# Kernel optimization log

Hardware: AMD Instinct MI355X
Metric: run time of the kernel (lower is better)

## Reference

```python
import jax, jax.numpy as jnp
import numpy as np

K = 16  # knn_graph k, loop=True (self included since d(i,i)=0 is minimal)


def _knn_idx(pos, k):
    # exact kNN via pairwise squared distances; [N, k] neighbor indices
    sq = jnp.sum(pos * pos, axis=-1)
    d2 = sq[:, None] + sq[None, :] - 2.0 * (pos @ pos.T)  # [N, N]
    _, idx = jax.lax.top_k(-d2, k)
    return idx


def _pointnet_conv(x, pos, idx, Wa, ba, Wb, bb):
    # PointNetConv: msg = MLP(concat(x_j, pos_j - pos_i)), max-aggregate over neighbors
    rel = pos[idx] - pos[:, None, :]                    # [N, K, 3]
    m = jnp.concatenate([x[idx], rel], axis=-1)          # [N, K, Cin+3]
    h = jax.nn.relu(m @ Wa + ba) @ Wb + bb               # [N, K, Cout]
    return jnp.max(h, axis=1)                            # [N, Cout]


def setup_inputs() -> dict:
    key = jax.random.key(0)
    ks = jax.random.split(key, 13)
    N = 8192
    c1, c2, c3 = 64, 64, 128
    s = lambda fi: 1.0 / np.sqrt(fi)
    pos = jax.random.normal(ks[0], (N, 3), dtype=jnp.float32)
    return {
        "pos": pos,
        "W1a": jax.random.normal(ks[1], (3 + 3, c1), jnp.float32) * s(6),
        "b1a": jnp.zeros((c1,), jnp.float32),
        "W1b": jax.random.normal(ks[2], (c1, c1), jnp.float32) * s(c1),
        "b1b": jnp.zeros((c1,), jnp.float32),
        "W2a": jax.random.normal(ks[3], (c1 + 3, c2), jnp.float32) * s(c1 + 3),
        "b2a": jnp.zeros((c2,), jnp.float32),
        "W2b": jax.random.normal(ks[4], (c2, c2), jnp.float32) * s(c2),
        "b2b": jnp.zeros((c2,), jnp.float32),
        "W3a": jax.random.normal(ks[5], (c2 + 3, c3), jnp.float32) * s(c2 + 3),
        "b3a": jnp.zeros((c3,), jnp.float32),
        "W3b": jax.random.normal(ks[6], (c3, c3), jnp.float32) * s(c3),
        "b3b": jnp.zeros((c3,), jnp.float32),
    }


def reference(pos, W1a, b1a, W1b, b1b, W2a, b2a, W2b, b2b, W3a, b3a, W3b, b3b):
    idx = _knn_idx(pos, K)
    h1 = jax.nn.relu(_pointnet_conv(pos, pos, idx, W1a, b1a, W1b, b1b))
    h2 = jax.nn.relu(_pointnet_conv(h1, pos, idx, W2a, b2a, W2b, b2b))
    h3 = jax.nn.relu(_pointnet_conv(h2, pos, idx, W3a, b3a, W3b, b3b))
    return (h1, h2, h3)
```

## Files before the change

kernel.cpp:

```cpp
#include <hip/hip_runtime.h>
#include <math.h>

#define N_PTS 8192
#define KNN 16

typedef __attribute__((ext_vector_type(8))) short bf16x8;
typedef __attribute__((ext_vector_type(4))) float f32x4v;

__device__ __forceinline__ unsigned short f2bf(float f)
{
    unsigned u = __float_as_uint(f);
    u = u + 0x7fffu + ((u >> 16) & 1u);
    return (unsigned short)(u >> 16);
}
__device__ __forceinline__ unsigned pack2(float a, float b)
{
    return (unsigned)f2bf(a) | ((unsigned)f2bf(b) << 16);
}
__device__ __forceinline__ float rfl(float x)
{
    return __int_as_float(__builtin_amdgcn_readfirstlane(__float_as_int(x)));
}

__global__ __launch_bounds__(256) void prep_kernel(const float* __restrict__ pos,
                                                   float4* __restrict__ pos4)
{
    const int i = blockIdx.x * 256 + threadIdx.x;
    const float x = pos[i * 3 + 0];
    const float y = pos[i * 3 + 1];
    const float z = pos[i * 3 + 2];
    pos4[i] = make_float4(x, y, z, fmaf(x, x, fmaf(y, y, z * z)));
}

__global__ __launch_bounds__(64) void prep_weights(
    const float* __restrict__ w1a, const float* __restrict__ w1b,
    const float* __restrict__ w2a, const float* __restrict__ w2b,
    const float* __restrict__ w3a, const float* __restrict__ w3b,
    uint4* __restrict__ dst)
{
    const float* Ws[6] = {w1a, w1b, w2a, w2b, w3a, w3b};
    const int Kd[6] = {6, 64, 67, 64, 67, 128};
    const int Nd[6] = {64, 64, 64, 64, 128, 128};
    const int start[7] = {0, 4, 12, 24, 32, 56, 88};

    const int b = blockIdx.x;
    int m = 0;
    while (b >= start[m + 1]) ++m;
    const int f  = b - start[m];
    const int NT = Nd[m] / 16;
    const int ks = f / NT, nt = f % NT;

    const int lane = threadIdx.x;
    const int c  = nt * 16 + (lane & 15);
    const int k0 = ks * 32 + (lane >> 4) * 8;
    const int K = Kd[m], N = Nd[m];
    const float* W = Ws[m];

    float v[8];
#pragma unroll
    for (int j = 0; j < 8; ++j) {
        const int kk = k0 + j;
        v[j] = (kk < K) ? W[kk * N + c] : 0.0f;
    }
    uint4 o;
    o.x = pack2(v[0], v[1]); o.y = pack2(v[2], v[3]);
    o.z = pack2(v[4], v[5]); o.w = pack2(v[6], v[7]);
    dst[b * 64 + lane] = o;
}

__device__ __forceinline__ unsigned sortkey(const float d2)
{
    unsigned u = __float_as_uint(d2);
    u ^= (unsigned)((int)u >> 31) | 0x80000000u;
    return u;
}

constexpr int CAP = 128;
constexpr int QB  = 8;
constexpr int QW  = QB / 4;

__global__ __launch_bounds__(256) void knn_kernel(const float4* __restrict__ pos4,
                                                  int* __restrict__ idx_out)
{
    __shared__ float mins[QB][4][64];
    __shared__ float Ts[QB];
    __shared__ unsigned long long surv[QB][CAP];
    __shared__ int scnt[QB];

    const int tid   = threadIdx.x;
    const int w     = tid >> 6;
    const int lane  = tid & 63;
    const int qbase = blockIdx.x * QB;
    const int cbase = w * (N_PTS / 4);

    if (tid < QB) scnt[tid] = 0;

    float qx[QB], qy[QB], qz[QB];
#pragma unroll
    for (int qi = 0; qi < QB; ++qi) {
        const float4 qp = pos4[qbase + qi];
        qx[qi] = rfl(-2.0f * qp.x);
        qy[qi] = rfl(-2.0f * qp.y);
        qz[qi] = rfl(-2.0f * qp.z);
    }

    float mn[QB];
#pragma unroll
    for (int qi = 0; qi < QB; ++qi) mn[qi] = 1e30f;

#pragma unroll 4
    for (int t = 0; t < N_PTS / 4 / 64; ++t) {
        const float4 p = pos4[cbase + t * 64 + lane];
#pragma unroll
        for (int qi = 0; qi < QB; ++qi) {
            const float s = fmaf(qx[qi], p.x, fmaf(qy[qi], p.y, fmaf(qz[qi], p.z, p.w)));
            mn[qi] = fminf(mn[qi], s);
        }
    }
#pragma unroll
    for (int qi = 0; qi < QB; ++qi) mins[qi][w][lane] = mn[qi];
    __syncthreads();

#pragma unroll
    for (int k = 0; k < QW; ++k) {
        const int q = w * QW + k;
        float v = fminf(fminf(mins[q][0][lane], mins[q][1][lane]),
                        fminf(mins[q][2][lane], mins[q][3][lane]));
#pragma unroll
        for (int kk = 2; kk <= 64; kk <<= 1)
#pragma unroll
            for (int j = kk >> 1; j > 0; j >>= 1) {
                const float o = __shfl_xor(v, j);
                const bool up = ((lane & kk) == 0);
                const bool lo = ((lane & j) == 0);
                v = (up == lo) ? fminf(v, o) : fmaxf(v, o);
            }
        if (lane == 15) Ts[q] = v;
    }
    __syncthreads();

    float T[QB];
#pragma unroll
    for (int qi = 0; qi < QB; ++qi) T[qi] = rfl(Ts[qi]);

#pragma unroll 4
    for (int t = 0; t < N_PTS / 4 / 64; ++t) {
        const int j = cbase + t * 64 + lane;
        const float4 p = pos4[j];
#pragma unroll
        for (int qi = 0; qi < QB; ++qi) {
            const float s = fmaf(qx[qi], p.x, fmaf(qy[qi], p.y, fmaf(qz[qi], p.z, p.w)));
            if (s <= T[qi]) {
                const int slot = atomicAdd(&scnt[qi], 1);
                if (slot < CAP)
                    surv[qi][slot] = ((unsigned long long)sortkey(s) << 32) | (unsigned)j;
            }
        }
    }
    __syncthreads();

    for (int k = 0; k < QW; ++k) {
        const int q = w * QW + k;
        const int n = min(scnt[q], CAP);
        const unsigned long long k0 = (lane < n) ? surv[q][lane] : ~0ull;
        const unsigned long long k1 = (lane + 64 < n) ? surv[q][lane + 64] : ~0ull;
        int r0 = 0, r1 = 0;
        for (int e = 0; e < n; ++e) {
            const unsigned long long ke = surv[q][e];
            r0 += (ke < k0) ? 1 : 0;
            r1 += (ke < k1) ? 1 : 0;
        }
        if (lane < n && r0 < KNN)
            idx_out[(qbase + q) * KNN + r0] = (int)(unsigned)(k0 & 0xFFFFFFFFu);
        if (lane + 64 < n && r1 < KNN)
            idx_out[(qbase + q) * KNN + r1] = (int)(unsigned)(k1 & 0xFFFFFFFFu);
    }
}

template <int CIN, int CMID, int COUT, int WM, int WN>
__global__ __launch_bounds__(256) void conv_mfma(
    const float* __restrict__ x, const float* __restrict__ pos,
    const int* __restrict__ idx,
    const uint4* __restrict__ fA, const float* __restrict__ ba,
    const uint4* __restrict__ fB, const float* __restrict__ bb,
    float* __restrict__ out)
{
    constexpr int PB  = 8, M = 128;
    constexpr int K1  = (CIN + 3 + 31) & ~31;
    constexpr int KS1 = K1 / 32;
    constexpr int KP1 = K1 + 8;
    constexpr int KS2 = CMID / 32;
    constexpr int KP2 = CMID + 8;
    constexpr int NT  = COUT / 16;
    constexpr int NTW = NT / WN;
    constexpr int MFW = (M / 16) / WM;

    __shared__ unsigned short msg[M][KP1];
    __shared__ unsigned short hbuf[M][KP2];
    __shared__ int nbr[M];

    const int tid  = threadIdx.x;
    const int lane = tid & 63;
    const int w    = tid >> 6;
    const int wm   = w / WN, wn = w % WN;
    const int i0   = blockIdx.x * PB;

    if (tid < M) nbr[tid] = idx[i0 * KNN + tid];
    __syncthreads();

    if constexpr (CIN == 3) {
        if (tid < M) {
            const int row = tid, p = row >> 4, j = nbr[row];
            const float ax = pos[j * 3 + 0], ay = pos[j * 3 + 1], az = pos[j * 3 + 2];
            const float bx = pos[(i0 + p) * 3 + 0], by = pos[(i0 + p) * 3 + 1],
                        bz = pos[(i0 + p) * 3 + 2];
            uint4 c0;
            c0.x = pack2(ax, ay);
            c0.y = pack2(az, ax - bx);
            c0.z = pack2(ay - by, az - bz);
            c0.w = 0u;
            *reinterpret_cast<uint4*>(&msg[row][0]) = c0;
            const uint4 z = make_uint4(0, 0, 0, 0);
            *reinterpret_cast<uint4*>(&msg[row][8])  = z;
            *reinterpret_cast<uint4*>(&msg[row][16]) = z;
            *reinterpret_cast<uint4*>(&msg[row][24]) = z;
        }
    } else {
        const int row = tid >> 1, hh = tid & 1;
        const int j = nbr[row];
        const float* xr = x + j * CIN + hh * 32;
#pragma unroll
        for (int cc = 0; cc < 32; cc += 8) {
            const float4 f0 = *reinterpret_cast<const float4*>(xr + cc);
            const float4 f1 = *reinterpret_cast<const float4*>(xr + cc + 4);
            uint4 o;
            o.x = pack2(f0.x, f0.y); o.y = pack2(f0.z, f0.w);
            o.z = pack2(f1.x, f1.y); o.w = pack2(f1.z, f1.w);
            *reinterpret_cast<uint4*>(&msg[row][hh * 32 + cc]) = o;
        }
        if (hh) {
            const int p = row >> 4;
            const float rx = pos[j * 3 + 0] - pos[(i0 + p) * 3 + 0];
            const float ry = pos[j * 3 + 1] - pos[(i0 + p) * 3 + 1];
            const float rz = pos[j * 3 + 2] - pos[(i0 + p) * 3 + 2];
            uint4 c0;
            c0.x = pack2(rx, ry);
            c0.y = pack2(rz, 0.0f);
            c0.z = 0u; c0.w = 0u;
            *reinterpret_cast<uint4*>(&msg[row][64]) = c0;
            const uint4 z = make_uint4(0, 0, 0, 0);
            *reinterpret_cast<uint4*>(&msg[row][72]) = z;
            *reinterpret_cast<uint4*>(&msg[row][80]) = z;
            *reinterpret_cast<uint4*>(&msg[row][88]) = z;
        }
    }
    __syncthreads();

    {
        uint4 b1[KS1][NTW];
#pragma unroll
        for (int ks = 0; ks < KS1; ++ks)
#pragma unroll
            for (int nt = 0; nt < NTW; ++nt)
                b1[ks][nt] = fA[(ks * NT + wn * NTW + nt) * 64 + lane];

        f32x4v acc[MFW][NTW];
#pragma unroll
        for (int mf = 0; mf < MFW; ++mf)
#pragma unroll
            for (int nt = 0; nt < NTW; ++nt) acc[mf][nt] = (f32x4v)0.0f;

#pragma unroll
        for (int mf = 0; mf < MFW; ++mf) {
            bf16x8 a[KS1];
#pragma unroll
            for (int ks = 0; ks < KS1; ++ks)
                a[ks] = *reinterpret_cast<const bf16x8*>(
                    &msg[(wm * MFW + mf) * 16 + (lane & 15)][ks * 32 + (lane >> 4) * 8]);
#pragma unroll
            for (int nt = 0; nt < NTW; ++nt)
#pragma unroll
                for (int ks = 0; ks < KS1; ++ks)
                    acc[mf][nt] = __builtin_amdgcn_mfma_f32_16x16x32_bf16(
                        a[ks], __builtin_bit_cast(bf16x8, b1[ks][nt]), acc[mf][nt], 0, 0, 0);
        }

        float bav[NTW];
#pragma unroll
        for (int nt = 0; nt < NTW; ++nt) bav[nt] = ba[(wn * NTW + nt) * 16 + (lane & 15)];

#pragma unroll
        for (int mf = 0; mf < MFW; ++mf)
#pragma unroll
            for (int nt = 0; nt < NTW; ++nt)
#pragma unroll
                for (int r = 0; r < 4; ++r) {
                    const float v = fmaxf(acc[mf][nt][r] + bav[nt], 0.0f);
                    hbuf[(wm * MFW + mf) * 16 + (lane >> 4) * 4 + r]
                        [(wn * NTW + nt) * 16 + (lane & 15)] = f2bf(v);
                }
    }
    __syncthreads();

    {
        uint4 b2[KS2][NTW];
#pragma unroll
        for (int ks = 0; ks < KS2; ++ks)
#pragma unroll
            for (int nt = 0; nt < NTW; ++nt)
                b2[ks][nt] = fB[(ks * NT + wn * NTW + nt) * 64 + lane];

        f32x4v acc[MFW][NTW];
#pragma unroll
        for (int mf = 0; mf < MFW; ++mf)
#pragma unroll
            for (int nt = 0; nt < NTW; ++nt) acc[mf][nt] = (f32x4v)0.0f;

#pragma unroll
        for (int mf = 0; mf < MFW; ++mf) {
            bf16x8 a[KS2];
#pragma unroll
            for (int ks = 0; ks < KS2; ++ks)
                a[ks] = *reinterpret_cast<const bf16x8*>(
                    &hbuf[(wm * MFW + mf) * 16 + (lane & 15)][ks * 32 + (lane >> 4) * 8]);
#pragma unroll
            for (int nt = 0; nt < NTW; ++nt)
#pragma unroll
                for (int ks = 0; ks < KS2; ++ks)
                    acc[mf][nt] = __builtin_amdgcn_mfma_f32_16x16x32_bf16(
                        a[ks], __builtin_bit_cast(bf16x8, b2[ks][nt]), acc[mf][nt], 0, 0, 0);
        }

        float bbv[NTW];
#pragma unroll
        for (int nt = 0; nt < NTW; ++nt) bbv[nt] = bb[(wn * NTW + nt) * 16 + (lane & 15)];

#pragma unroll
        for (int mf = 0; mf < MFW; ++mf)
#pragma unroll
            for (int nt = 0; nt < NTW; ++nt) {
                const f32x4v t = acc[mf][nt];
                float m0 = fmaxf(fmaxf(t[0], t[1]), fmaxf(t[2], t[3]));
                m0 = fmaxf(m0, __shfl_xor(m0, 16));
                m0 = fmaxf(m0, __shfl_xor(m0, 32));
                const float v = fmaxf(m0 + bbv[nt], 0.0f);
                if (lane < 16)
                    out[(i0 + wm * MFW + mf) * COUT + (wn * NTW + nt) * 16 + lane] = v;
            }
    }
}

extern "C" void kernel_launch(void* const* d_in, const int* in_sizes, int n_in,
                              void* d_out, int out_size, void* d_ws, size_t ws_size,
                              hipStream_t stream)
{
    const float* pos = (const float*)d_in[0];
    const float* W1a = (const float*)d_in[1];
    const float* b1a = (const float*)d_in[2];
    const float* W1b = (const float*)d_in[3];
    const float* b1b = (const float*)d_in[4];
    const float* W2a = (const float*)d_in[5];
    const float* b2a = (const float*)d_in[6];
    const float* W2b = (const float*)d_in[7];
    const float* b2b = (const float*)d_in[8];
    const float* W3a = (const float*)d_in[9];
    const float* b3a = (const float*)d_in[10];
    const float* W3b = (const float*)d_in[11];
    const float* b3b = (const float*)d_in[12];

    float* out = (float*)d_out;
    float* h1 = out;
    float* h2 = out + N_PTS * 64;
    float* h3 = out + N_PTS * 128;

    int*   idx     = (int*)d_ws;
    uint4* wsFrags = (uint4*)((char*)d_ws + N_PTS * KNN * 4);

    float4* pos4 = (float4*)h3;

    prep_weights<<<88, 64, 0, stream>>>(W1a, W1b, W2a, W2b, W3a, W3b, wsFrags);
    prep_kernel<<<N_PTS / 256, 256, 0, stream>>>(pos, pos4);
    knn_kernel<<<N_PTS / QB, 256, 0, stream>>>(pos4, idx);

    const uint4* fW1a = wsFrags + 0 * 64;
    const uint4* fW1b = wsFrags + 4 * 64;
    const uint4* fW2a = wsFrags + 12 * 64;
    const uint4* fW2b = wsFrags + 24 * 64;
    const uint4* fW3a = wsFrags + 32 * 64;
    const uint4* fW3b = wsFrags + 56 * 64;

    conv_mfma<3, 64, 64, 4, 1><<<N_PTS / 8, 256, 0, stream>>>(
        pos, pos, idx, fW1a, b1a, fW1b, b1b, h1);
    conv_mfma<64, 64, 64, 4, 1><<<N_PTS / 8, 256, 0, stream>>>(
        h1, pos, idx, fW2a, b2a, fW2b, b2b, h2);
    conv_mfma<64, 128, 128, 2, 2><<<N_PTS / 8, 256, 0, stream>>>(
        h2, pos, idx, fW3a, b3a, fW3b, b3b, h3);
}
```

Baseline: 78.55 us.

## Merge prep kernels, double kNN query batch, prefetch candidates, alias conv LDS buffers

Combines the weight-fragment and pos4 prep kernels into one launch to save a kernel launch. Raises the kNN queries per block from 8 to 16 so each candidate load is reused across more queries, and software-prefetches candidate points four at a time in both kNN passes. In the conv kernel the msg and hbuf LDS arrays share one buffer, separated by an extra barrier, which cuts LDS use and may raise occupancy. The larger query batch adds register pressure and halves the kNN grid size.

```diff
diff --git a/kernel.cpp b/kernel.cpp
--- a/kernel.cpp
+++ b/kernel.cpp
@@ -22,50 +22,47 @@
     return __int_as_float(__builtin_amdgcn_readfirstlane(__float_as_int(x)));
 }
 
-__global__ __launch_bounds__(256) void prep_kernel(const float* __restrict__ pos,
-                                                   float4* __restrict__ pos4)
-{
-    const int i = blockIdx.x * 256 + threadIdx.x;
-    const float x = pos[i * 3 + 0];
-    const float y = pos[i * 3 + 1];
-    const float z = pos[i * 3 + 2];
-    pos4[i] = make_float4(x, y, z, fmaf(x, x, fmaf(y, y, z * z)));
-}
-
-__global__ __launch_bounds__(64) void prep_weights(
+__global__ __launch_bounds__(256) void prep_all(
+    const float* __restrict__ pos, float4* __restrict__ pos4,
     const float* __restrict__ w1a, const float* __restrict__ w1b,
     const float* __restrict__ w2a, const float* __restrict__ w2b,
     const float* __restrict__ w3a, const float* __restrict__ w3b,
     uint4* __restrict__ dst)
 {
-    const float* Ws[6] = {w1a, w1b, w2a, w2b, w3a, w3b};
-    const int Kd[6] = {6, 64, 67, 64, 67, 128};
-    const int Nd[6] = {64, 64, 64, 64, 128, 128};
-    const int start[7] = {0, 4, 12, 24, 32, 56, 88};
-
     const int b = blockIdx.x;
-    int m = 0;
-    while (b >= start[m + 1]) ++m;
-    const int f  = b - start[m];
-    const int NT = Nd[m] / 16;
-    const int ks = f / NT, nt = f % NT;
-
-    const int lane = threadIdx.x;
-    const int c  = nt * 16 + (lane & 15);
-    const int k0 = ks * 32 + (lane >> 4) * 8;
-    const int K = Kd[m], N = Nd[m];
-    const float* W = Ws[m];
-
-    float v[8];
-#pragma unroll
-    for (int j = 0; j < 8; ++j) {
-        const int kk = k0 + j;
-        v[j] = (kk < K) ? W[kk * N + c] : 0.0f;
-    }
-    uint4 o;
-    o.x = pack2(v[0], v[1]); o.y = pack2(v[2], v[3]);
-    o.z = pack2(v[4], v[5]); o.w = pack2(v[6], v[7]);
-    dst[b * 64 + lane] = o;
+    if (b < 88) {
+        if (threadIdx.x >= 64) return;
+        const float* Ws[6] = {w1a, w1b, w2a, w2b, w3a, w3b};
+        const int Kd[6] = {6, 64, 67, 64, 67, 128};
+        const int Nd[6] = {64, 64, 64, 64, 128, 128};
+        const int start[7] = {0, 4, 12, 24, 32, 56, 88};
+        int m = 0;
+        while (b >= start[m + 1]) ++m;
+        const int f  = b - start[m];
+        const int NT = Nd[m] / 16;
+        const int ks = f / NT, nt = f % NT;
+        const int lane = threadIdx.x;
+        const int c  = nt * 16 + (lane & 15);
+        const int k0 = ks * 32 + (lane >> 4) * 8;
+        const int K = Kd[m], N = Nd[m];
+        const float* W = Ws[m];
+        float v[8];
+#pragma unroll
+        for (int j = 0; j < 8; ++j) {
+            const int kk = k0 + j;
+            v[j] = (kk < K) ? W[kk * N + c] : 0.0f;
+        }
+        uint4 o;
+        o.x = pack2(v[0], v[1]); o.y = pack2(v[2], v[3]);
+        o.z = pack2(v[4], v[5]); o.w = pack2(v[6], v[7]);
+        dst[b * 64 + lane] = o;
+    } else {
+        const int i = (b - 88) * 256 + threadIdx.x;
+        const float x = pos[i * 3 + 0];
+        const float y = pos[i * 3 + 1];
+        const float z = pos[i * 3 + 2];
+        pos4[i] = make_float4(x, y, z, fmaf(x, x, fmaf(y, y, z * z)));
+    }
 }
 
 __device__ __forceinline__ unsigned sortkey(const float d2)
@@ -76,7 +73,7 @@
 }
 
 constexpr int CAP = 128;
-constexpr int QB  = 8;
+constexpr int QB  = 16;
 constexpr int QW  = QB / 4;
 
 __global__ __launch_bounds__(256) void knn_kernel(const float4* __restrict__ pos4,
@@ -108,13 +105,31 @@
 #pragma unroll
     for (int qi = 0; qi < QB; ++qi) mn[qi] = 1e30f;
 
-#pragma unroll 4
-    for (int t = 0; t < N_PTS / 4 / 64; ++t) {
-        const float4 p = pos4[cbase + t * 64 + lane];
+    const float4* cp = pos4 + cbase + lane;
+
+    {
+        float4 c0 = cp[0 * 64], c1 = cp[1 * 64], c2 = cp[2 * 64], c3 = cp[3 * 64];
+#pragma unroll 1
+        for (int t = 0; t < 28; t += 4) {
+            const float4 n0 = cp[(t + 4) * 64];
+            const float4 n1 = cp[(t + 5) * 64];
+            const float4 n2 = cp[(t + 6) * 64];
+            const float4 n3 = cp[(t + 7) * 64];
+#pragma unroll
+            for (int qi = 0; qi < QB; ++qi) {
+                mn[qi] = fminf(mn[qi], fmaf(qx[qi], c0.x, fmaf(qy[qi], c0.y, fmaf(qz[qi], c0.z, c0.w))));
+                mn[qi] = fminf(mn[qi], fmaf(qx[qi], c1.x, fmaf(qy[qi], c1.y, fmaf(qz[qi], c1.z, c1.w))));
+                mn[qi] = fminf(mn[qi], fmaf(qx[qi], c2.x, fmaf(qy[qi], c2.y, fmaf(qz[qi], c2.z, c2.w))));
+                mn[qi] = fminf(mn[qi], fmaf(qx[qi], c3.x, fmaf(qy[qi], c3.y, fmaf(qz[qi], c3.z, c3.w))));
+            }
+            c0 = n0; c1 = n1; c2 = n2; c3 = n3;
+        }
 #pragma unroll
         for (int qi = 0; qi < QB; ++qi) {
-            const float s = fmaf(qx[qi], p.x, fmaf(qy[qi], p.y, fmaf(qz[qi], p.z, p.w)));
-            mn[qi] = fminf(mn[qi], s);
+            mn[qi] = fminf(mn[qi], fmaf(qx[qi], c0.x, fmaf(qy[qi], c0.y, fmaf(qz[qi], c0.z, c0.w))));
+            mn[qi] = fminf(mn[qi], fmaf(qx[qi], c1.x, fmaf(qy[qi], c1.y, fmaf(qz[qi], c1.z, c1.w))));
+            mn[qi] = fminf(mn[qi], fmaf(qx[qi], c2.x, fmaf(qy[qi], c2.y, fmaf(qz[qi], c2.z, c2.w))));
+            mn[qi] = fminf(mn[qi], fmaf(qx[qi], c3.x, fmaf(qy[qi], c3.y, fmaf(qz[qi], c3.z, c3.w))));
         }
     }
 #pragma unroll
@@ -143,18 +158,30 @@
 #pragma unroll
     for (int qi = 0; qi < QB; ++qi) T[qi] = rfl(Ts[qi]);
 
-#pragma unroll 4
-    for (int t = 0; t < N_PTS / 4 / 64; ++t) {
-        const int j = cbase + t * 64 + lane;
-        const float4 p = pos4[j];
-#pragma unroll
-        for (int qi = 0; qi < QB; ++qi) {
-            const float s = fmaf(qx[qi], p.x, fmaf(qy[qi], p.y, fmaf(qz[qi], p.z, p.w)));
-            if (s <= T[qi]) {
-                const int slot = atomicAdd(&scnt[qi], 1);
-                if (slot < CAP)
-                    surv[qi][slot] = ((unsigned long long)sortkey(s) << 32) | (unsigned)j;
+    {
+        float4 c0 = cp[0 * 64], c1 = cp[1 * 64], c2 = cp[2 * 64], c3 = cp[3 * 64];
+#pragma unroll 1
+        for (int t = 0; t < 32; t += 4) {
+            float4 n0, n1, n2, n3;
+            if (t + 4 < 32) {
+                n0 = cp[(t + 4) * 64]; n1 = cp[(t + 5) * 64];
+                n2 = cp[(t + 6) * 64]; n3 = cp[(t + 7) * 64];
             }
+#pragma unroll
+            for (int u = 0; u < 4; ++u) {
+                const float4 p = (u == 0) ? c0 : (u == 1) ? c1 : (u == 2) ? c2 : c3;
+                const int j = cbase + (t + u) * 64 + lane;
+#pragma unroll
+                for (int qi = 0; qi < QB; ++qi) {
+                    const float s = fmaf(qx[qi], p.x, fmaf(qy[qi], p.y, fmaf(qz[qi], p.z, p.w)));
+                    if (s <= T[qi]) {
+                        const int slot = atomicAdd(&scnt[qi], 1);
+                        if (slot < CAP)
+                            surv[qi][slot] = ((unsigned long long)sortkey(s) << 32) | (unsigned)j;
+                    }
+                }
+            }
+            if (t + 4 < 32) { c0 = n0; c1 = n1; c2 = n2; c3 = n3; }
         }
     }
     __syncthreads();
@@ -194,10 +221,12 @@
     constexpr int NT  = COUT / 16;
     constexpr int NTW = NT / WN;
     constexpr int MFW = (M / 16) / WM;
-
-    __shared__ unsigned short msg[M][KP1];
-    __shared__ unsigned short hbuf[M][KP2];
+    constexpr int MSGS = M * KP1;
+    constexpr int HBS  = M * KP2;
+    constexpr int BUFS = (MSGS > HBS) ? MSGS : HBS;
+
     __shared__ int nbr[M];
+    __shared__ __align__(16) unsigned short buf[BUFS];
 
     const int tid  = threadIdx.x;
     const int lane = tid & 63;
@@ -219,11 +248,11 @@
             c0.y = pack2(az, ax - bx);
             c0.z = pack2(ay - by, az - bz);
             c0.w = 0u;
-            *reinterpret_cast<uint4*>(&msg[row][0]) = c0;
+            *reinterpret_cast<uint4*>(&buf[row * KP1 + 0])  = c0;
             const uint4 z = make_uint4(0, 0, 0, 0);
-            *reinterpret_cast<uint4*>(&msg[row][8])  = z;
-            *reinterpret_cast<uint4*>(&msg[row][16]) = z;
-            *reinterpret_cast<uint4*>(&msg[row][24]) = z;
+            *reinterpret_cast<uint4*>(&buf[row * KP1 + 8])  = z;
+            *reinterpret_cast<uint4*>(&buf[row * KP1 + 16]) = z;
+            *reinterpret_cast<uint4*>(&buf[row * KP1 + 24]) = z;
         }
     } else {
         const int row = tid >> 1, hh = tid & 1;
@@ -236,7 +265,7 @@
             uint4 o;
             o.x = pack2(f0.x, f0.y); o.y = pack2(f0.z, f0.w);
             o.z = pack2(f1.x, f1.y); o.w = pack2(f1.z, f1.w);
-            *reinterpret_cast<uint4*>(&msg[row][hh * 32 + cc]) = o;
+            *reinterpret_cast<uint4*>(&buf[row * KP1 + hh * 32 + cc]) = o;
         }
         if (hh) {
             const int p = row >> 4;
@@ -247,15 +276,16 @@
             c0.x = pack2(rx, ry);
             c0.y = pack2(rz, 0.0f);
             c0.z = 0u; c0.w = 0u;
-            *reinterpret_cast<uint4*>(&msg[row][64]) = c0;
+            *reinterpret_cast<uint4*>(&buf[row * KP1 + 64]) = c0;
             const uint4 z = make_uint4(0, 0, 0, 0);
-            *reinterpret_cast<uint4*>(&msg[row][72]) = z;
-            *reinterpret_cast<uint4*>(&msg[row][80]) = z;
-            *reinterpret_cast<uint4*>(&msg[row][88]) = z;
-        }
-    }
-    __syncthreads();
-
+            *reinterpret_cast<uint4*>(&buf[row * KP1 + 72]) = z;
+            *reinterpret_cast<uint4*>(&buf[row * KP1 + 80]) = z;
+            *reinterpret_cast<uint4*>(&buf[row * KP1 + 88]) = z;
+        }
+    }
+    __syncthreads();
+
+    f32x4v acc[MFW][NTW];
     {
         uint4 b1[KS1][NTW];
 #pragma unroll
@@ -264,7 +294,6 @@
             for (int nt = 0; nt < NTW; ++nt)
                 b1[ks][nt] = fA[(ks * NT + wn * NTW + nt) * 64 + lane];
 
-        f32x4v acc[MFW][NTW];
 #pragma unroll
         for (int mf = 0; mf < MFW; ++mf)
 #pragma unroll
@@ -276,7 +305,7 @@
 #pragma unroll
             for (int ks = 0; ks < KS1; ++ks)
                 a[ks] = *reinterpret_cast<const bf16x8*>(
-                    &msg[(wm * MFW + mf) * 16 + (lane & 15)][ks * 32 + (lane >> 4) * 8]);
+                    &buf[((wm * MFW + mf) * 16 + (lane & 15)) * KP1 + ks * 32 + (lane >> 4) * 8]);
 #pragma unroll
             for (int nt = 0; nt < NTW; ++nt)
 #pragma unroll
@@ -284,11 +313,13 @@
                     acc[mf][nt] = __builtin_amdgcn_mfma_f32_16x16x32_bf16(
                         a[ks], __builtin_bit_cast(bf16x8, b1[ks][nt]), acc[mf][nt], 0, 0, 0);
         }
-
+    }
+    __syncthreads();
+
+    {
         float bav[NTW];
 #pragma unroll
         for (int nt = 0; nt < NTW; ++nt) bav[nt] = ba[(wn * NTW + nt) * 16 + (lane & 15)];
-
 #pragma unroll
         for (int mf = 0; mf < MFW; ++mf)
 #pragma unroll
@@ -296,8 +327,8 @@
 #pragma unroll
                 for (int r = 0; r < 4; ++r) {
                     const float v = fmaxf(acc[mf][nt][r] + bav[nt], 0.0f);
-                    hbuf[(wm * MFW + mf) * 16 + (lane >> 4) * 4 + r]
-                        [(wn * NTW + nt) * 16 + (lane & 15)] = f2bf(v);
+                    buf[((wm * MFW + mf) * 16 + (lane >> 4) * 4 + r) * KP2 +
+                        (wn * NTW + nt) * 16 + (lane & 15)] = f2bf(v);
                 }
     }
     __syncthreads();
@@ -310,11 +341,11 @@
             for (int nt = 0; nt < NTW; ++nt)
                 b2[ks][nt] = fB[(ks * NT + wn * NTW + nt) * 64 + lane];
 
-        f32x4v acc[MFW][NTW];
+        f32x4v acc2[MFW][NTW];
 #pragma unroll
         for (int mf = 0; mf < MFW; ++mf)
 #pragma unroll
-            for (int nt = 0; nt < NTW; ++nt) acc[mf][nt] = (f32x4v)0.0f;
+            for (int nt = 0; nt < NTW; ++nt) acc2[mf][nt] = (f32x4v)0.0f;
 
 #pragma unroll
         for (int mf = 0; mf < MFW; ++mf) {
@@ -322,13 +353,13 @@
 #pragma unroll
             for (int ks = 0; ks < KS2; ++ks)
                 a[ks] = *reinterpret_cast<const bf16x8*>(
-                    &hbuf[(wm * MFW + mf) * 16 + (lane & 15)][ks * 32 + (lane >> 4) * 8]);
+                    &buf[((wm * MFW + mf) * 16 + (lane & 15)) * KP2 + ks * 32 + (lane >> 4) * 8]);
 #pragma unroll
             for (int nt = 0; nt < NTW; ++nt)
 #pragma unroll
                 for (int ks = 0; ks < KS2; ++ks)
-                    acc[mf][nt] = __builtin_amdgcn_mfma_f32_16x16x32_bf16(
-                        a[ks], __builtin_bit_cast(bf16x8, b2[ks][nt]), acc[mf][nt], 0, 0, 0);
+                    acc2[mf][nt] = __builtin_amdgcn_mfma_f32_16x16x32_bf16(
+                        a[ks], __builtin_bit_cast(bf16x8, b2[ks][nt]), acc2[mf][nt], 0, 0, 0);
         }
 
         float bbv[NTW];
@@ -339,7 +370,7 @@
         for (int mf = 0; mf < MFW; ++mf)
 #pragma unroll
             for (int nt = 0; nt < NTW; ++nt) {
-                const f32x4v t = acc[mf][nt];
+                const f32x4v t = acc2[mf][nt];
                 float m0 = fmaxf(fmaxf(t[0], t[1]), fmaxf(t[2], t[3]));
                 m0 = fmaxf(m0, __shfl_xor(m0, 16));
                 m0 = fmaxf(m0, __shfl_xor(m0, 32));
@@ -378,8 +409,7 @@
 
     float4* pos4 = (float4*)h3;
 
-    prep_weights<<<88, 64, 0, stream>>>(W1a, W1b, W2a, W2b, W3a, W3b, wsFrags);
-    prep_kernel<<<N_PTS / 256, 256, 0, stream>>>(pos, pos4);
+    prep_all<<<120, 256, 0, stream>>>(pos, pos4, W1a, W1b, W2a, W2b, W3a, W3b, wsFrags);
     knn_kernel<<<N_PTS / QB, 256, 0, stream>>>(pos4, idx);
 
     const uint4* fW1a = wsFrags + 0 * 64;
```

After: 84.19 us. 7.2% more time.
